# Performance work log

Measured on AMD Instinct MI355X. Metric: run time of the kernel, lower is better.

## Reference

```python
import jax, jax.numpy as jnp
import numpy as np

# Mamba2 config (matches mamba_ssm.Mamba2 defaults used by the wrapper)
D_MODEL = 1024
D_STATE = 128
D_CONV = 4
EXPAND = 2
HEADDIM = 64
CHUNK = 256
D_INNER = EXPAND * D_MODEL            # 2048
NHEADS = D_INNER // HEADDIM           # 32
CONV_DIM = D_INNER + 2 * D_STATE      # 2304 (x, B, C share the causal conv)
D_IN_PROJ = 2 * D_INNER + 2 * D_STATE + NHEADS  # z, xBC, dt
EPS = 1e-5


def rmsnorm(x, w, eps=EPS):
    return x * jax.lax.rsqrt(jnp.mean(x * x, axis=-1, keepdims=True) + eps) * w


def setup_inputs() -> dict:
    key = jax.random.key(0)
    ks = jax.random.split(key, 8)
    B, L = 2, 2048
    def w(k, shape, sc=0.02):
        return jax.random.normal(k, shape, jnp.float32) * sc
    return {
        "x": jax.random.normal(ks[0], (B, L, D_MODEL), jnp.float32),
        "norm_w": jnp.ones((D_MODEL,), jnp.float32),
        "in_proj_w": w(ks[1], (D_IN_PROJ, D_MODEL)),
        "conv_w": w(ks[2], (CONV_DIM, 1, D_CONV), 0.2),   # depthwise kernel
        "conv_b": jnp.zeros((CONV_DIM,), jnp.float32),
        "dt_bias": w(ks[3], (NHEADS,), 1.0),
        "A_log": jnp.log(1.0 + 15.0 * jax.random.uniform(ks[4], (NHEADS,), jnp.float32)),
        "D": jnp.ones((NHEADS,), jnp.float32),
        "gnorm_w": jnp.ones((D_INNER,), jnp.float32),
        "out_proj_w": w(ks[5], (D_MODEL, D_INNER)),
    }


def _ssd(xd, a, Bm, Cm):
    """Chunked SSD scan (ssd_minimal_discrete).
    xd: (b,l,h,p) = x*dt ; a: (b,l,h) = dt*A ; Bm,Cm: (b,l,n) (ngroups=1)."""
    b, l, h, p = xd.shape
    n = Bm.shape[-1]
    nc = l // CHUNK
    xd = xd.reshape(b, nc, CHUNK, h, p)
    a = a.reshape(b, nc, CHUNK, h).transpose(0, 3, 1, 2)   # (b,h,nc,c)
    Bm = Bm.reshape(b, nc, CHUNK, n)
    Cm = Cm.reshape(b, nc, CHUNK, n)
    a_cs = jnp.cumsum(a, axis=-1)                           # (b,h,nc,c)
    # 1) intra-chunk: causal decay matrix L[t,s] = exp(sum_{s<i<=t} a_i)
    diff = a_cs[..., :, None] - a_cs[..., None, :]          # (b,h,nc,c,c)
    mask = jnp.tril(jnp.ones((CHUNK, CHUNK), bool))
    Lm = jnp.exp(jnp.where(mask, diff, 0.0)) * mask
    Y_diag = jnp.einsum("bcln,bcsn,bhcls,bcshp->bclhp", Cm, Bm, Lm, xd)
    # 2) per-chunk end states
    decay_states = jnp.exp(a_cs[..., -1:] - a_cs)           # (b,h,nc,c)
    states = jnp.einsum("bcln,bhcl,bclhp->bchpn", Bm, decay_states, xd)
    # 3) inter-chunk recurrence (vectorized segsum over the 8+1 chunk totals)
    tot = jnp.pad(a_cs[..., -1], ((0, 0), (0, 0), (1, 0)))  # (b,h,nc+1)
    tot_cs = jnp.cumsum(tot, axis=-1)
    dchunk = tot_cs[..., :, None] - tot_cs[..., None, :]    # (b,h,nc+1,nc+1)
    cmask = jnp.tril(jnp.ones((nc + 1, nc + 1), bool))
    dchunk = jnp.exp(jnp.where(cmask, dchunk, 0.0)) * cmask
    states = jnp.concatenate([jnp.zeros_like(states[:, :1]), states], axis=1)
    new_states = jnp.einsum("bhzc,bchpn->bzhpn", dchunk, states)
    init_states = new_states[:, :-1]                        # state entering each chunk
    # 4) state -> output contribution
    Y_off = jnp.einsum("bcln,bchpn,bhcl->bclhp", Cm, init_states, jnp.exp(a_cs))
    return (Y_diag + Y_off).reshape(b, l, h, p)


def reference(x, norm_w, in_proj_w, conv_w, conv_b, dt_bias, A_log, D, gnorm_w, out_proj_w):
    res = x
    u = rmsnorm(x, norm_w)
    zxbcdt = u @ in_proj_w.T                                # (b,l,d_in_proj)
    z, xBC, dt = jnp.split(zxbcdt, [D_INNER, D_INNER + CONV_DIM], axis=-1)
    # causal depthwise conv1d over (x,B,C), then SiLU
    xBC_t = jnp.pad(xBC.transpose(0, 2, 1), ((0, 0), (0, 0), (D_CONV - 1, 0)))
    conv = jax.lax.conv_general_dilated(
        xBC_t, conv_w, (1,), "VALID",
        dimension_numbers=("NCH", "OIH", "NCH"), feature_group_count=CONV_DIM)
    xBC = jax.nn.silu(conv.transpose(0, 2, 1) + conv_b)
    xs, Bm, Cm = jnp.split(xBC, [D_INNER, D_INNER + D_STATE], axis=-1)
    dt = jax.nn.softplus(dt + dt_bias)                      # (b,l,h)
    A = -jnp.exp(A_log)                                     # (h,)
    xh = xs.reshape(xs.shape[0], xs.shape[1], NHEADS, HEADDIM)
    y = _ssd(xh * dt[..., None], dt * A, Bm, Cm)
    y = y + D[None, None, :, None] * xh                     # skip term
    y = y.reshape(xs.shape)
    y = rmsnorm(y * jax.nn.silu(z), gnorm_w)                # gated RMSNorm
    return res + y @ out_proj_w.T
```

## Files before the change

### kernel.cpp

```cpp
#include <hip/hip_runtime.h>
#include <hip/hip_bf16.h>

typedef __hip_bfloat16 bf16_t;
typedef __attribute__((ext_vector_type(8))) short bfrag8;
typedef __attribute__((ext_vector_type(4))) float floatx4;

#define DM     1024
#define DI     2048
#define NHD    32
#define HD     64
#define DSTATE 128
#define CONVD  2304
#define NPROJ  4384
#define NPAD   4480
#define MR     4096
#define LL     2048
#define EPSF   1e-5f
#define LOG2E  1.44269504088896f

__device__ __forceinline__ void gl_lds16(const void* g, void* l) {
  __builtin_amdgcn_global_load_lds((const __attribute__((address_space(1))) void*)g,
                                   (__attribute__((address_space(3))) void*)l, 16, 0, 0);
}
__device__ __forceinline__ unsigned pack_bf16_rn(float a, float b) {
  unsigned ua = (__float_as_uint(a) + 0x8000u) >> 16;
  unsigned ub = (__float_as_uint(b) + 0x8000u) >> 16;
  return ua | (ub << 16);
}
__device__ __forceinline__ unsigned short bf16u(float a) {
  return (unsigned short)((__float_as_uint(a) + 0x8000u) >> 16);
}
__device__ __forceinline__ float blo(unsigned u){ return __uint_as_float(u << 16); }
__device__ __forceinline__ float bhi(unsigned u){ return __uint_as_float(u & 0xffff0000u); }
__device__ __forceinline__ void unp8(uint4 u, float* v) {
  v[0]=blo(u.x); v[1]=bhi(u.x); v[2]=blo(u.y); v[3]=bhi(u.y);
  v[4]=blo(u.z); v[5]=bhi(u.z); v[6]=blo(u.w); v[7]=bhi(u.w);
}
typedef union { unsigned u[4]; bfrag8 f; } fragu;

__global__ void rms1_kernel(const float* __restrict__ x, const float* __restrict__ w,
                            bf16_t* __restrict__ ub) {
  int row = blockIdx.x, t = threadIdx.x;
  float4 v = ((const float4*)(x + (long)row * DM))[t];
  float ss = v.x*v.x + v.y*v.y + v.z*v.z + v.w*v.w;
#pragma unroll
  for (int off = 32; off > 0; off >>= 1) ss += __shfl_down(ss, off, 64);
  __shared__ float red[4];
  if ((t & 63) == 0) red[t >> 6] = ss;
  __syncthreads();
  float tot = red[0] + red[1] + red[2] + red[3];
  float rs = rsqrtf(tot * (1.f / DM) + EPSF);
  float4 wv = ((const float4*)w)[t];
  bf16_t* o = ub + (long)row * DM + t * 4;
  o[0] = __float2bfloat16(v.x * rs * wv.x);
  o[1] = __float2bfloat16(v.y * rs * wv.y);
  o[2] = __float2bfloat16(v.z * rs * wv.z);
  o[3] = __float2bfloat16(v.w * rs * wv.w);
}

#define W1CNT (NPAD * DM / 4)
#define W2CNT (DM * DI / 4)
__global__ void cvtw_kernel(const float* __restrict__ w1, const float* __restrict__ w2,
                            const float* __restrict__ gw,
                            bf16_t* __restrict__ o1, bf16_t* __restrict__ o2) {
  int i4 = blockIdx.x * 256 + threadIdx.x;
  if (i4 < W1CNT) {
    int idx = i4 * 4;
    int row = idx >> 10;
    float4 v = make_float4(0.f, 0.f, 0.f, 0.f);
    if (row < NPROJ) v = *(const float4*)(w1 + idx);
    bf16_t* d = o1 + idx;
    d[0] = __float2bfloat16(v.x); d[1] = __float2bfloat16(v.y);
    d[2] = __float2bfloat16(v.z); d[3] = __float2bfloat16(v.w);
  } else {
    int idx = (i4 - W1CNT) * 4;
    int k = idx & (DI - 1);
    float4 v = *(const float4*)(w2 + idx);
    float4 g = *(const float4*)(gw + k);
    bf16_t* d = o2 + idx;
    d[0] = __float2bfloat16(v.x * g.x); d[1] = __float2bfloat16(v.y * g.y);
    d[2] = __float2bfloat16(v.z * g.z); d[3] = __float2bfloat16(v.w * g.w);
  }
}

template<int TN, bool DO_RES, bool OUT_BF16>
__global__ __launch_bounds__(256) void gemm64_kernel(const bf16_t* __restrict__ A,
    const bf16_t* __restrict__ Bw, const float* __restrict__ resid,
    const float* __restrict__ rs_row, void* __restrict__ Cout, int N, int K) {
  __shared__ bf16_t As[128 * 64];
  __shared__ bf16_t Bs[TN * 64];
  const int tid = threadIdx.x;
  const int lane = tid & 63;
  const int wv = tid >> 6;
  const int l15 = lane & 15;
  const int l4 = lane >> 4;
  constexpr int MF = (TN == 128) ? 4 : 2;
  const int wm = (TN == 128) ? ((wv >> 1) << 6) : (wv << 5);
  const int wn = (TN == 128) ? ((wv & 1) << 6) : 0;
  const int tm = blockIdx.x << 7;
  const int tn = blockIdx.y * TN;

  floatx4 acc[MF][4];
#pragma unroll
  for (int i = 0; i < MF; i++)
#pragma unroll
    for (int j = 0; j < 4; j++) acc[i][j] = (floatx4){0.f, 0.f, 0.f, 0.f};

  const int r = tid >> 3;
  const int c8 = tid & 7;
  const int scol = ((c8 ^ (r & 7)) << 3);
  const bf16_t* Ag = A + (long)(tm + r) * K + scol;
  const bf16_t* Bg = Bw + (long)(tn + r) * K + scol;
  const int swz = l15 & 7;

  for (int k0 = 0; k0 < K; k0 += 64) {
#pragma unroll
    for (int q = 0; q < 4; q++)
      gl_lds16(Ag + (long)(q * 32) * K + k0, &As[q * 2048 + tid * 8]);
#pragma unroll
    for (int q = 0; q < TN / 32; q++)
      gl_lds16(Bg + (long)(q * 32) * K + k0, &Bs[q * 2048 + tid * 8]);
    __syncthreads();
#pragma unroll
    for (int kk = 0; kk < 2; kk++) {
      bfrag8 af[MF], bfr[4];
      const int ch = ((kk << 2) | l4) ^ swz;
#pragma unroll
      for (int j = 0; j < 4; j++)
        bfr[j] = *(const bfrag8*)&Bs[(wn + j * 16 + l15) * 64 + ch * 8];
#pragma unroll
      for (int i = 0; i < MF; i++)
        af[i] = *(const bfrag8*)&As[(wm + i * 16 + l15) * 64 + ch * 8];
#pragma unroll
      for (int i = 0; i < MF; i++)
#pragma unroll
        for (int j = 0; j < 4; j++)
          acc[i][j] = __builtin_amdgcn_mfma_f32_16x16x32_bf16(af[i], bfr[j], acc[i][j], 0, 0, 0);
    }
    __syncthreads();
  }
#pragma unroll
  for (int i = 0; i < MF; i++)
#pragma unroll
    for (int j = 0; j < 4; j++)
#pragma unroll
      for (int r2 = 0; r2 < 4; r2++) {
        int row = tm + wm + i * 16 + l4 * 4 + r2;
        int col = tn + wn + j * 16 + l15;
        float v = acc[i][j][r2];
        if (OUT_BF16) {
          ((bf16_t*)Cout)[(long)row * N + col] = __float2bfloat16(v);
        } else {
          if (DO_RES) v = v * rs_row[row] + resid[(long)row * N + col];
          ((float*)Cout)[(long)row * N + col] = v;
        }
      }
}

__global__ __launch_bounds__(512, 2) void gemm256_kernel(const bf16_t* __restrict__ A,
    const bf16_t* __restrict__ Bw, bf16_t* __restrict__ Cout) {
  __shared__ bf16_t lds[65536];
  const int t = threadIdx.x;
  const int lane = t & 63, wv = t >> 6;
  const int wm = wv >> 2, wn = wv & 3;
  const int l15 = lane & 15, l4 = lane >> 4;
  const int flat = blockIdx.x;
  const int swzb = (flat & 7) * 32 + (flat >> 3);
  const int bx = swzb & 15, by = swzb >> 4;
  const int tm = bx << 8, tn = by << 8;

  const int srow = t >> 3;
  const int scol = ((t & 7) ^ (srow & 7)) << 3;
  const bf16_t* Ag = A + (long)(tm + srow) * DM + scol;
  const bf16_t* Bg = Bw + (long)(tn + srow) * DM + scol;
  bf16_t* Asl = lds;
  bf16_t* Bsl = lds + 32768;
  const int swl = (l15 & 7) << 4;
  const int ca0 = (l4 * 16) ^ swl;
  const int ca1 = (64 + l4 * 16) ^ swl;

  floatx4 acc[8][4];
#pragma unroll
  for (int i = 0; i < 8; i++)
#pragma unroll
    for (int j = 0; j < 4; j++) acc[i][j] = (floatx4){0.f, 0.f, 0.f, 0.f};
  bfrag8 bq[8];

#define STG_A(tt, h) { \
  bf16_t* d_ = Asl + (((tt) & 1) * 2 + (h)) * 8192 + t * 8; \
  gl_lds16(Ag + (long)((h) * 128     ) * DM + (tt) * 64, d_); \
  gl_lds16(Ag + (long)((h) * 128 + 64) * DM + (tt) * 64, d_ + 4096); \
}
#define STG_B(tt, h) { \
  bf16_t* d_ = Bsl + (((tt) & 1) * 2 + (h)) * 8192 + t * 8; \
  gl_lds16(Bg + (long)((h) * 128     ) * DM + (tt) * 64, d_); \
  gl_lds16(Bg + (long)((h) * 128 + 64) * DM + (tt) * 64, d_ + 4096); \
}
#define PH(d, q, STG, WT) { \
  const char* Ah_ = (const char*)(Asl + ((d) * 2 + wm) * 8192); \
  const char* Bh_ = (const char*)(Bsl + ((d) * 2 + (wn >> 1)) * 8192); \
  if ((q) == 0) { \
    _Pragma("unroll") \
    for (int j = 0; j < 4; j++) { \
      int r_ = ((wn & 1) << 6) + j * 16 + l15; \
      bq[j * 2]     = *(const bfrag8*)(Bh_ + r_ * 128 + ca0); \
      bq[j * 2 + 1] = *(const bfrag8*)(Bh_ + r_ * 128 + ca1); \
    } \
  } \
  bfrag8 aq0, aq1, aq2, aq3; \
  { int r_ = (q) * 32 + l15; \
    aq0 = *(const bfrag8*)(Ah_ + r_ * 128 + ca0); \
    aq1 = *(const bfrag8*)(Ah_ + r_ * 128 + ca1); \
    aq2 = *(const bfrag8*)(Ah_ + (r_ + 16) * 128 + ca0); \
    aq3 = *(const bfrag8*)(Ah_ + (r_ + 16) * 128 + ca1); } \
  STG; \
  __builtin_amdgcn_s_barrier(); \
  asm volatile("s_waitcnt lgkmcnt(0)" ::: "memory"); \
  __builtin_amdgcn_s_setprio(1); \
  _Pragma("unroll") \
  for (int j = 0; j < 4; j++) { \
    acc[(q)*2  ][j] = __builtin_amdgcn_mfma_f32_16x16x32_bf16(aq0, bq[j*2],   acc[(q)*2  ][j], 0, 0, 0); \
    acc[(q)*2  ][j] = __builtin_amdgcn_mfma_f32_16x16x32_bf16(aq1, bq[j*2+1], acc[(q)*2  ][j], 0, 0, 0); \
    acc[(q)*2+1][j] = __builtin_amdgcn_mfma_f32_16x16x32_bf16(aq2, bq[j*2],   acc[(q)*2+1][j], 0, 0, 0); \
    acc[(q)*2+1][j] = __builtin_amdgcn_mfma_f32_16x16x32_bf16(aq3, bq[j*2+1], acc[(q)*2+1][j], 0, 0, 0); \
  } \
  __builtin_amdgcn_s_setprio(0); \
  WT; \
  __builtin_amdgcn_s_barrier(); \
}

  STG_A(0, 0); STG_A(0, 1); STG_B(0, 0); STG_B(0, 1);
  STG_B(1, 0); STG_B(1, 1);
  asm volatile("s_waitcnt vmcnt(4)" ::: "memory");
  __builtin_amdgcn_s_barrier();

  for (int it = 0; it < 7; ++it) {
    const int ta = 2 * it, tb = ta + 1;
    PH(0, 0, STG_A(tb, 0), {})
    PH(0, 1, STG_A(tb, 1), {})
    PH(0, 2, STG_B(ta + 2, 0), {})
    PH(0, 3, STG_B(ta + 2, 1), asm volatile("s_waitcnt vmcnt(4)" ::: "memory");)
    PH(1, 0, STG_A(ta + 2, 0), {})
    PH(1, 1, STG_A(ta + 2, 1), {})
    PH(1, 2, STG_B(tb + 2, 0), {})
    PH(1, 3, STG_B(tb + 2, 1), asm volatile("s_waitcnt vmcnt(4)" ::: "memory");)
  }
  {
    PH(0, 0, STG_A(15, 0), {})
    PH(0, 1, STG_A(15, 1), {})
    PH(0, 2, {}, {})
    PH(0, 3, {}, asm volatile("s_waitcnt vmcnt(0)" ::: "memory");)
    PH(1, 0, {}, {})
    PH(1, 1, {}, {})
    PH(1, 2, {}, {})
    PH(1, 3, {}, {})
  }
#undef PH
#undef STG_A
#undef STG_B

  const long crow = tm + wm * 128;
  const int ccol = tn + wn * 64;
#pragma unroll
  for (int qi = 0; qi < 8; qi++)
#pragma unroll
    for (int j = 0; j < 4; j++)
#pragma unroll
      for (int r2 = 0; r2 < 4; r2++) {
        long row = crow + (qi >> 1) * 32 + (qi & 1) * 16 + l4 * 4 + r2;
        int col = ccol + j * 16 + l15;
        Cout[row * NPAD + col] = __float2bfloat16(acc[qi][j][r2]);
      }
}

__global__ __launch_bounds__(256) void gemm_s_kernel(const bf16_t* __restrict__ Cmh,
                const bf16_t* __restrict__ Bmh, float* __restrict__ SL) {
  __shared__ bf16_t As[128 * 32];
  __shared__ bf16_t Bs[128 * 32];
  const int tid = threadIdx.x;
  const int lane = tid & 63;
  const int wv = tid >> 6;
  const int wm = (wv >> 1) << 6;
  const int wn = (wv & 1) << 6;
  const int bc = blockIdx.z;
  const int tm = blockIdx.x << 7;
  const int tn = blockIdx.y << 7;
  const int l15 = lane & 15;
  const int l4 = lane >> 4;
  floatx4 acc[4][4];
#pragma unroll
  for (int i = 0; i < 4; i++)
#pragma unroll
    for (int j = 0; j < 4; j++) acc[i][j] = (floatx4){0.f, 0.f, 0.f, 0.f};
  const int arow = tid >> 2;
  const int acol = (tid & 3) << 3;
  const bf16_t* Ag = Cmh + (long)bc * 256 * DSTATE + (long)(tm + arow) * DSTATE + acol;
  const bf16_t* Bg = Bmh + (long)bc * 256 * DSTATE + (long)(tn + arow) * DSTATE + acol;
  const long k64 = (long)64 * DSTATE;
  for (int k0 = 0; k0 < DSTATE; k0 += 32) {
    gl_lds16(Ag + k0, &As[tid * 8]);
    gl_lds16(Ag + k64 + k0, &As[2048 + tid * 8]);
    gl_lds16(Bg + k0, &Bs[tid * 8]);
    gl_lds16(Bg + k64 + k0, &Bs[2048 + tid * 8]);
    __syncthreads();
    bfrag8 af[4], bfr[4];
#pragma unroll
    for (int i = 0; i < 4; i++)
      af[i] = *(const bfrag8*)&As[(wm + i * 16 + l15) * 32 + l4 * 8];
#pragma unroll
    for (int j = 0; j < 4; j++)
      bfr[j] = *(const bfrag8*)&Bs[(wn + j * 16 + l15) * 32 + l4 * 8];
#pragma unroll
    for (int i = 0; i < 4; i++)
#pragma unroll
      for (int j = 0; j < 4; j++)
        acc[i][j] = __builtin_amdgcn_mfma_f32_16x16x32_bf16(af[i], bfr[j], acc[i][j], 0, 0, 0);
    __syncthreads();
  }
  float* Cb = SL + (long)bc * 65536;
#pragma unroll
  for (int i = 0; i < 4; i++)
#pragma unroll
    for (int j = 0; j < 4; j++)
#pragma unroll
      for (int r = 0; r < 4; r++)
        Cb[(long)(tm + wm + i * 16 + l4 * 4 + r) * 256 + tn + wn + j * 16 + l15] = acc[i][j][r];
}

__global__ __launch_bounds__(256) void conv4_kernel(const bf16_t* __restrict__ zxh,
    const float* __restrict__ cw, const float* __restrict__ cb,
    bf16_t* __restrict__ xhb, bf16_t* __restrict__ Bmh, bf16_t* __restrict__ Cmh) {
  int g = blockIdx.x * 256 + threadIdx.x;
  int cg = g % 288;
  int blt = g / 288;
  int c0 = cg * 8;
  long bl0 = (long)blt * 4;
  int l0 = (int)(bl0 & (LL - 1));
  const bf16_t* base = zxh + bl0 * NPAD + DI + c0;
  float rv[7][8];
#pragma unroll
  for (int j = 0; j < 7; j++) {
    int dj = j - 3;
    if (l0 + dj >= 0) {
      uint4 u = *(const uint4*)(base + (long)dj * NPAD);
      unp8(u, rv[j]);
    } else {
#pragma unroll
      for (int q = 0; q < 8; q++) rv[j][q] = 0.f;
    }
  }
  float4 wq[8];
#pragma unroll
  for (int q = 0; q < 8; q++) wq[q] = ((const float4*)cw)[c0 + q];
  float bias[8];
  *(float4*)&bias[0] = *(const float4*)(cb + c0);
  *(float4*)&bias[4] = *(const float4*)(cb + c0 + 4);
#pragma unroll
  for (int i = 0; i < 4; i++) {
    unsigned o[4];
#pragma unroll
    for (int q2 = 0; q2 < 4; q2++) {
      float rr[2];
#pragma unroll
      for (int e = 0; e < 2; e++) {
        int q = q2 * 2 + e;
        float a = bias[q] + wq[q].x * rv[i][q] + wq[q].y * rv[i + 1][q]
                + wq[q].z * rv[i + 2][q] + wq[q].w * rv[i + 3][q];
        rr[e] = a / (1.f + __expf(-a));
      }
      o[q2] = pack_bf16_rn(rr[0], rr[1]);
    }
    uint4 ov = make_uint4(o[0], o[1], o[2], o[3]);
    long bl = bl0 + i;
    if (c0 < DI)               *(uint4*)(xhb + bl * DI + c0) = ov;
    else if (c0 < DI + DSTATE) *(uint4*)(Bmh + bl * DSTATE + (c0 - DI)) = ov;
    else                       *(uint4*)(Cmh + bl * DSTATE + (c0 - DI - DSTATE)) = ov;
  }
}

__global__ __launch_bounds__(256) void xdt_kernel(const bf16_t* __restrict__ xhb,
    const bf16_t* __restrict__ Bmh, const bf16_t* __restrict__ zxh,
    const float* __restrict__ A_log, const float* __restrict__ dtb,
    float* __restrict__ acs, float* __restrict__ ctot,
    bf16_t* __restrict__ xdT, bf16_t* __restrict__ xdTe, bf16_t* __restrict__ BmT) {
  __shared__ unsigned short Tb[9216];
  __shared__ float acsL[256];
  __shared__ float dtsL[256];
  __shared__ float wsum[4];
  int blk = blockIdx.x;
  int t = threadIdx.x;
  if (blk < 512) {
    int h = blk & 31, bc = blk >> 5;
    {
      int lane = t & 63, w = t >> 6;
      float Ah = -__expf(A_log[h]) * LOG2E;
      int gl = bc * 256 + t;
      float vv = __bfloat162float(zxh[(long)gl * NPAD + (NPROJ - 32) + h]) + dtb[h];
      float sp = fmaxf(vv, 0.f) + log1pf(__expf(-fabsf(vv)));
      float a = sp * Ah;
#pragma unroll
      for (int off = 1; off < 64; off <<= 1) {
        float v = __shfl_up(a, off, 64);
        if (lane >= off) a += v;
      }
      if (lane == 63) wsum[w] = a;
      __syncthreads();
      float base = 0.f;
      for (int i = 0; i < 4; i++) base += (i < w) ? wsum[i] : 0.f;
      a += base;
      acsL[t] = a;
      dtsL[t] = sp;
      acs[blk * 256 + t] = a;
      if (t == 255) ctot[blk] = a;
      __syncthreads();
    }
    float atot = acsL[255];
    unsigned short* T1 = Tb;
    unsigned short* T2 = Tb + 4608;
    int l_loc = t >> 2, pg = t & 3;
    for (int lt = 0; lt < 4; lt++) {
      int ll = lt * 64 + l_loc;
      int gl = bc * 256 + ll;
      float w1 = dtsL[ll];
      float w2 = w1 * exp2f(atot - acsL[ll]);
      const uint4* src = (const uint4*)(xhb + (long)gl * DI + h * HD + pg * 16);
      uint4 u0 = src[0], u1 = src[1];
      float v[16];
      unp8(u0, v); unp8(u1, v + 8);
      __syncthreads();
#pragma unroll
      for (int q = 0; q < 16; q++) {
        T1[(pg * 16 + q) * 72 + l_loc] = bf16u(v[q] * w1);
        T2[(pg * 16 + q) * 72 + l_loc] = bf16u(v[q] * w2);
      }
      __syncthreads();
      long orow = ((long)blk * 64 + l_loc) * 256 + lt * 64 + pg * 16;
      *(uint4*)(xdT + orow)      = *(uint4*)&T1[l_loc * 72 + pg * 16];
      *(uint4*)(xdT + orow + 8)  = *(uint4*)&T1[l_loc * 72 + pg * 16 + 8];
      *(uint4*)(xdTe + orow)     = *(uint4*)&T2[l_loc * 72 + pg * 16];
      *(uint4*)(xdTe + orow + 8) = *(uint4*)&T2[l_loc * 72 + pg * 16 + 8];
    }
  } else {
    unsigned short* T = Tb;
    int bc = blk - 512;
    int l_loc = t >> 2, ng = t & 3;
    for (int lt = 0; lt < 4; lt++) {
      int gl = bc * 256 + lt * 64 + l_loc;
      const uint4* src = (const uint4*)(Bmh + (long)gl * DSTATE + ng * 32);
      uint4 u[4];
#pragma unroll
      for (int q = 0; q < 4; q++) u[q] = src[q];
      __syncthreads();
      const unsigned short* us = (const unsigned short*)u;
#pragma unroll
      for (int e = 0; e < 32; e++)
        T[(ng * 32 + e) * 72 + l_loc] = us[e];
      __syncthreads();
      int n = t >> 1, lg2 = t & 1;
      long orow = ((long)bc * 128 + n) * 256 + lt * 64 + lg2 * 32;
#pragma unroll
      for (int q = 0; q < 4; q++)
        *(uint4*)(BmT + orow + q * 8) = *(uint4*)&T[n * 72 + lg2 * 32 + q * 8];
    }
  }
}

__global__ __launch_bounds__(256) void states3_kernel(const bf16_t* __restrict__ xdTe,
    const bf16_t* __restrict__ BmT, bf16_t* __restrict__ states) {
  int blk = blockIdx.x;
  int bc = blk >> 5;
  int t = threadIdx.x, lane = t & 63, wv = t >> 6;
  int l15 = lane & 15, l4 = lane >> 4;
  floatx4 acc[2][4];
#pragma unroll
  for (int i = 0; i < 2; i++)
#pragma unroll
    for (int j = 0; j < 4; j++) acc[i][j] = (floatx4){0.f, 0.f, 0.f, 0.f};
  const bf16_t* arow = BmT + (long)bc * 128 * 256;
  const bf16_t* brow = xdTe + (long)blk * 64 * 256;
#pragma unroll
  for (int kt = 0; kt < 8; kt++) {
    bfrag8 af[2], bfr[4];
#pragma unroll
    for (int i = 0; i < 2; i++)
      af[i] = *(const bfrag8*)(arow + (long)(wv * 32 + i * 16 + l15) * 256 + kt * 32 + l4 * 8);
#pragma unroll
    for (int j = 0; j < 4; j++)
      bfr[j] = *(const bfrag8*)(brow + (long)(j * 16 + l15) * 256 + kt * 32 + l4 * 8);
#pragma unroll
    for (int i = 0; i < 2; i++)
#pragma unroll
      for (int j = 0; j < 4; j++)
        acc[i][j] = __builtin_amdgcn_mfma_f32_16x16x32_bf16(af[i], bfr[j], acc[i][j], 0, 0, 0);
  }
#pragma unroll
  for (int i = 0; i < 2; i++)
#pragma unroll
    for (int j = 0; j < 4; j++) {
      int n_base = wv * 32 + i * 16 + l4 * 4;
      int p = j * 16 + l15;
      unsigned lo = pack_bf16_rn(acc[i][j][0], acc[i][j][1]);
      unsigned hi = pack_bf16_rn(acc[i][j][2], acc[i][j][3]);
      *(uint2*)(states + (long)blk * 8192 + p * 128 + n_base) = make_uint2(lo, hi);
    }
}

__global__ void scan_kernel(const bf16_t* __restrict__ states, const float* __restrict__ ctot,
                            bf16_t* __restrict__ initsb) {
  int id = blockIdx.x * 256 + threadIdx.x;
  int pn = id & 8191;
  int bh = id >> 13;
  int b = bh >> 5, h = bh & 31;
  float S = 0.f;
#pragma unroll
  for (int c = 0; c < 8; c++) {
    int blk = (b * 8 + c) * 32 + h;
    initsb[(long)blk * 8192 + pn] = __float2bfloat16(S);
    S = exp2f(ctot[blk]) * S + __bfloat162float(states[(long)blk * 8192 + pn]);
  }
}

__global__ __launch_bounds__(512, 4) void yk4_kernel(const float* __restrict__ SL,
     const bf16_t* __restrict__ Cmh, const bf16_t* __restrict__ xhb,
     const bf16_t* __restrict__ zxh, const float* __restrict__ acs,
     const bf16_t* __restrict__ initsb, const bf16_t* __restrict__ xdT,
     const float* __restrict__ Dp, bf16_t* __restrict__ yg, float* __restrict__ ssqp) {
  int bi = blockIdx.x;
  int bc = (bi & 7) * 2 + ((bi >> 3) & 1);
  int h = bi >> 4;
  int ablk = bc * 32 + h;
  int t = threadIdx.x;
  int wv = t >> 6;
  int mh = wv >> 2, wsub = wv & 3;
  int lane = t & 63;
  int l15 = lane & 15, l4 = lane >> 4;

  __shared__ float acsS[256];
  __shared__ __align__(16) char bbuf[49152];
  bf16_t* xds = (bf16_t*)bbuf;
  bf16_t* ins = (bf16_t*)(bbuf + 32768);
  float* Yt = (float*)bbuf;

  {
    const bf16_t* xrow_g = xdT + (long)ablk * 64 * 256;
#pragma unroll
    for (int it = 0; it < 4; it++) {
      int sl = it * 512 + t;
      int p = sl >> 5, s = sl & 31;
      int c = (s & 24) | ((s & 7) ^ (p & 7));
      gl_lds16(xrow_g + p * 256 + c * 8, &xds[sl * 8]);
    }
    const bf16_t* irow_g = initsb + (long)ablk * 8192;
#pragma unroll
    for (int it = 0; it < 2; it++) {
      int sl = it * 512 + t;
      int p = sl >> 4, s = sl & 15;
      int c = (s & 8) | ((s & 7) ^ (p & 7));
      gl_lds16(irow_g + p * 128 + c * 8, &ins[sl * 8]);
    }
  }
  if (t < 256) acsS[t] = acs[ablk * 256 + t];
  __syncthreads();

  const int rowbase = bc * 256;
  const int l0 = mh * 128 + wsub * 32 + l15;
  const int l1 = l0 + 16;
  const float al0 = acsS[l0], al1 = acsS[l1];
  const float eA0 = exp2f(al0), eA1 = exp2f(al1);
  const float* SL0 = SL + (long)bc * 65536 + (long)l0 * 256;
  const float* SL1 = SL + (long)bc * 65536 + (long)l1 * 256;

  floatx4 acc[2][4];
#pragma unroll
  for (int i = 0; i < 2; i++)
#pragma unroll
    for (int j = 0; j < 4; j++) acc[i][j] = (floatx4){0.f, 0.f, 0.f, 0.f};

  const int nkd = (mh + 1) * 4;
  for (int kt = 0; kt < nkd; kt++) {
    int sbase = kt * 32 + l4 * 8;
    float as[8];
    *(float4*)&as[0] = *(const float4*)&acsS[sbase];
    *(float4*)&as[4] = *(const float4*)&acsS[sbase + 4];
    float sv0[8], sv1[8];
    *(float4*)&sv0[0] = *(const float4*)(SL0 + sbase);
    *(float4*)&sv0[4] = *(const float4*)(SL0 + sbase + 4);
    *(float4*)&sv1[0] = *(const float4*)(SL1 + sbase);
    *(float4*)&sv1[4] = *(const float4*)(SL1 + sbase + 4);
    fragu af0, af1;
#pragma unroll
    for (int q2 = 0; q2 < 4; q2++) {
      float p00, p01, p10, p11;
      {
        int s = sbase + q2 * 2;
        float d0 = al0 - as[q2 * 2], d1 = al0 - as[q2 * 2 + 1];
        p00 = (s <= l0) ? sv0[q2 * 2] * exp2f(fminf(d0, 0.f)) : 0.f;
        p01 = (s + 1 <= l0) ? sv0[q2 * 2 + 1] * exp2f(fminf(d1, 0.f)) : 0.f;
        float e0 = al1 - as[q2 * 2], e1 = al1 - as[q2 * 2 + 1];
        p10 = (s <= l1) ? sv1[q2 * 2] * exp2f(fminf(e0, 0.f)) : 0.f;
        p11 = (s + 1 <= l1) ? sv1[q2 * 2 + 1] * exp2f(fminf(e1, 0.f)) : 0.f;
      }
      af0.u[q2] = pack_bf16_rn(p00, p01);
      af1.u[q2] = pack_bf16_rn(p10, p11);
    }
    bfrag8 bfr[4];
    int ch = kt * 4 + l4;
#pragma unroll
    for (int j = 0; j < 4; j++) {
      int p = j * 16 + l15;
      int sw = (ch & 24) | ((ch & 7) ^ (p & 7));
      bfr[j] = *(const bfrag8*)&xds[(p * 32 + sw) * 8];
    }
#pragma unroll
    for (int j = 0; j < 4; j++) {
      acc[0][j] = __builtin_amdgcn_mfma_f32_16x16x32_bf16(af0.f, bfr[j], acc[0][j], 0, 0, 0);
      acc[1][j] = __builtin_amdgcn_mfma_f32_16x16x32_bf16(af1.f, bfr[j], acc[1][j], 0, 0, 0);
    }
  }
#pragma unroll
  for (int kt = 0; kt < 4; kt++) {
    int n0 = kt * 32 + l4 * 8;
    uint4 c0 = *(const uint4*)(Cmh + (long)(rowbase + l0) * DSTATE + n0);
    uint4 c1 = *(const uint4*)(Cmh + (long)(rowbase + l1) * DSTATE + n0);
    float cv0[8], cv1[8];
    unp8(c0, cv0); unp8(c1, cv1);
    fragu af0, af1;
#pragma unroll
    for (int q2 = 0; q2 < 4; q2++) {
      af0.u[q2] = pack_bf16_rn(cv0[q2 * 2] * eA0, cv0[q2 * 2 + 1] * eA0);
      af1.u[q2] = pack_bf16_rn(cv1[q2 * 2] * eA1, cv1[q2 * 2 + 1] * eA1);
    }
    bfrag8 bfr[4];
    int ch = kt * 4 + l4;
#pragma unroll
    for (int j = 0; j < 4; j++) {
      int p = j * 16 + l15;
      int sw = (ch & 8) | ((ch & 7) ^ (p & 7));
      bfr[j] = *(const bfrag8*)&ins[(p * 16 + sw) * 8];
    }
#pragma unroll
    for (int j = 0; j < 4; j++) {
      acc[0][j] = __builtin_amdgcn_mfma_f32_16x16x32_bf16(af0.f, bfr[j], acc[0][j], 0, 0, 0);
      acc[1][j] = __builtin_amdgcn_mfma_f32_16x16x32_bf16(af1.f, bfr[j], acc[1][j], 0, 0, 0);
    }
  }
  float Dh = Dp[h];
#pragma unroll
  for (int pass = 0; pass < 2; pass++) {
    __syncthreads();
    if (mh == pass) {
#pragma unroll
      for (int i = 0; i < 2; i++)
#pragma unroll
        for (int j = 0; j < 4; j++)
#pragma unroll
          for (int r = 0; r < 4; r++)
            Yt[(wsub * 32 + i * 16 + l4 * 4 + r) * 66 + j * 16 + l15] = acc[i][j][r];
    }
    __syncthreads();
    {
      int row_l = t >> 2;
      int chc = (t & 3) * 16;
      long rowg = rowbase + pass * 128 + row_l;
      float ss = 0.f;
#pragma unroll
      for (int it = 0; it < 2; it++) {
        int c = chc + it * 8;
        float4 y0 = *(const float4*)&Yt[row_l * 66 + c];
        float4 y1 = *(const float4*)&Yt[row_l * 66 + c + 4];
        uint4 ux = *(const uint4*)(xhb + rowg * DI + h * HD + c);
        uint4 uz = *(const uint4*)(zxh + rowg * NPAD + h * HD + c);
        float xv[8], zv[8];
        unp8(ux, xv); unp8(uz, zv);
        float yv[8] = {y0.x, y0.y, y0.z, y0.w, y1.x, y1.y, y1.z, y1.w};
        unsigned o[4];
#pragma unroll
        for (int q = 0; q < 4; q++) {
          float v0 = (yv[q * 2 + 0] + Dh * xv[q * 2 + 0]) *
                     (zv[q * 2 + 0] / (1.f + __expf(-zv[q * 2 + 0])));
          float v1 = (yv[q * 2 + 1] + Dh * xv[q * 2 + 1]) *
                     (zv[q * 2 + 1] / (1.f + __expf(-zv[q * 2 + 1])));
          ss += v0 * v0 + v1 * v1;
          o[q] = pack_bf16_rn(v0, v1);
        }
        *(uint4*)(yg + rowg * DI + h * HD + c) = make_uint4(o[0], o[1], o[2], o[3]);
      }
      ss += __shfl_xor(ss, 1, 64);
      ss += __shfl_xor(ss, 2, 64);
      if ((t & 3) == 0) ssqp[rowg * 32 + h] = ss;
    }
  }
}

__global__ void rsred_kernel(const float* __restrict__ ssqp, float* __restrict__ rs) {
  int row = blockIdx.x * 256 + threadIdx.x;
  const float4* p = (const float4*)(ssqp + row * 32);
  float s = 0.f;
#pragma unroll
  for (int q = 0; q < 8; q++) {
    float4 v = p[q];
    s += v.x + v.y + v.z + v.w;
  }
  rs[row] = rsqrtf(s * (1.f / DI) + EPSF);
}

extern "C" void kernel_launch(void* const* d_in, const int* in_sizes, int n_in,
                              void* d_out, int out_size, void* d_ws, size_t ws_size,
                              hipStream_t stream) {
  const float* x    = (const float*)d_in[0];
  const float* nw   = (const float*)d_in[1];
  const float* w1   = (const float*)d_in[2];
  const float* cw   = (const float*)d_in[3];
  const float* cb   = (const float*)d_in[4];
  const float* dtb  = (const float*)d_in[5];
  const float* alog = (const float*)d_in[6];
  const float* Dp   = (const float*)d_in[7];
  const float* gw   = (const float*)d_in[8];
  const float* w2   = (const float*)d_in[9];
  float* out = (float*)d_out;

  char* ws = (char*)d_ws;
  size_t off = 0;
  auto alloc = [&](size_t bytes) -> void* {
    void* p = ws + off;
    off += (bytes + 255) & ~(size_t)255;
    return p;
  };
  bf16_t* ub     = (bf16_t*)alloc((size_t)MR * DM * 2);
  bf16_t* w1b    = (bf16_t*)alloc((size_t)NPAD * DM * 2);
  bf16_t* w2b    = (bf16_t*)alloc((size_t)DM * DI * 2);
  bf16_t* zxh    = (bf16_t*)alloc((size_t)MR * NPAD * 2);
  bf16_t* xhb    = (bf16_t*)alloc((size_t)MR * DI * 2);
  bf16_t* Bmh    = (bf16_t*)alloc((size_t)MR * DSTATE * 2);
  bf16_t* Cmh    = (bf16_t*)alloc((size_t)MR * DSTATE * 2);
  float* SL      = (float*)alloc((size_t)16 * 256 * 256 * 4);
  float* acs     = (float*)alloc((size_t)512 * 256 * 4);
  float* ctot    = (float*)alloc((size_t)512 * 4);
  bf16_t* states = (bf16_t*)alloc((size_t)512 * 8192 * 2);
  bf16_t* initsb = (bf16_t*)alloc((size_t)512 * 8192 * 2);
  bf16_t* xdT    = (bf16_t*)alloc((size_t)512 * 64 * 256 * 2);
  bf16_t* xdTe   = (bf16_t*)alloc((size_t)512 * 64 * 256 * 2);
  bf16_t* BmT    = (bf16_t*)alloc((size_t)16 * 128 * 256 * 2);
  bf16_t* yg     = (bf16_t*)alloc((size_t)MR * DI * 2);
  float* ssqp    = (float*)alloc((size_t)MR * NHD * 4);
  float* rs      = (float*)alloc((size_t)MR * 4);
  if (off > ws_size) return;

  rms1_kernel<<<MR, 256, 0, stream>>>(x, nw, ub);
  cvtw_kernel<<<(W1CNT + W2CNT) / 256, 256, 0, stream>>>(w1, w2, gw, w1b, w2b);
  gemm256_kernel<<<256, 512, 0, stream>>>(ub, w1b, zxh);
  gemm64_kernel<64, false, true><<<dim3(MR / 128, 6), 256, 0, stream>>>(
      ub, w1b + (size_t)4096 * DM, nullptr, nullptr, zxh + 4096, NPAD, DM);
  conv4_kernel<<<(1024 * 288) / 256, 256, 0, stream>>>(zxh, cw, cb, xhb, Bmh, Cmh);
  xdt_kernel<<<528, 256, 0, stream>>>(xhb, Bmh, zxh, alog, dtb, acs, ctot, xdT, xdTe, BmT);
  gemm_s_kernel<<<dim3(2, 2, 16), 256, 0, stream>>>(Cmh, Bmh, SL);
  states3_kernel<<<512, 256, 0, stream>>>(xdTe, BmT, states);
  scan_kernel<<<(2 * 32 * 8192) / 256, 256, 0, stream>>>(states, ctot, initsb);
  yk4_kernel<<<512, 512, 0, stream>>>(SL, Cmh, xhb, zxh, acs, initsb, xdT, Dp, yg, ssqp);
  rsred_kernel<<<MR / 256, 256, 0, stream>>>(ssqp, rs);
  gemm64_kernel<64, true, false><<<dim3(MR / 128, DM / 64), 256, 0, stream>>>(
      yg, w2b, x, rs, out, DM, DI);
}
```

Before: 263.7 us.

## Merge small kernels, fold rms reduction into out-proj GEMM, retile GEMMs

Merges rmsnorm with the weight conversion, and the states GEMM with the C·B score GEMM, each into a single launch. The gated-RMSNorm row reduction moves into the out-projection GEMM prologue, which removes the separate reduction kernel. Both small GEMMs switch to 128-wide N tiles, and the main GEMM gets a new XCD-aware block mapping. The aim is to cut launch count and gaps between launches and to improve cache locality, at the cost of fewer blocks in the retiled GEMMs. Each out-proj block now recomputes the row reduction redundantly.

```diff
diff --git a/kernel.cpp b/kernel.cpp
--- a/kernel.cpp
+++ b/kernel.cpp
@@ -38,57 +38,61 @@
 }
 typedef union { unsigned u[4]; bfrag8 f; } fragu;
 
-__global__ void rms1_kernel(const float* __restrict__ x, const float* __restrict__ w,
-                            bf16_t* __restrict__ ub) {
-  int row = blockIdx.x, t = threadIdx.x;
-  float4 v = ((const float4*)(x + (long)row * DM))[t];
-  float ss = v.x*v.x + v.y*v.y + v.z*v.z + v.w*v.w;
-#pragma unroll
-  for (int off = 32; off > 0; off >>= 1) ss += __shfl_down(ss, off, 64);
-  __shared__ float red[4];
-  if ((t & 63) == 0) red[t >> 6] = ss;
-  __syncthreads();
-  float tot = red[0] + red[1] + red[2] + red[3];
-  float rs = rsqrtf(tot * (1.f / DM) + EPSF);
-  float4 wv = ((const float4*)w)[t];
-  bf16_t* o = ub + (long)row * DM + t * 4;
-  o[0] = __float2bfloat16(v.x * rs * wv.x);
-  o[1] = __float2bfloat16(v.y * rs * wv.y);
-  o[2] = __float2bfloat16(v.z * rs * wv.z);
-  o[3] = __float2bfloat16(v.w * rs * wv.w);
-}
-
 #define W1CNT (NPAD * DM / 4)
 #define W2CNT (DM * DI / 4)
-__global__ void cvtw_kernel(const float* __restrict__ w1, const float* __restrict__ w2,
-                            const float* __restrict__ gw,
-                            bf16_t* __restrict__ o1, bf16_t* __restrict__ o2) {
-  int i4 = blockIdx.x * 256 + threadIdx.x;
-  if (i4 < W1CNT) {
-    int idx = i4 * 4;
-    int row = idx >> 10;
-    float4 v = make_float4(0.f, 0.f, 0.f, 0.f);
-    if (row < NPROJ) v = *(const float4*)(w1 + idx);
-    bf16_t* d = o1 + idx;
-    d[0] = __float2bfloat16(v.x); d[1] = __float2bfloat16(v.y);
-    d[2] = __float2bfloat16(v.z); d[3] = __float2bfloat16(v.w);
+#define CVTBLK ((W1CNT + W2CNT) / 256)
+__global__ void rms_cvt_kernel(const float* __restrict__ x, const float* __restrict__ w,
+                               bf16_t* __restrict__ ub,
+                               const float* __restrict__ w1, const float* __restrict__ w2,
+                               const float* __restrict__ gw,
+                               bf16_t* __restrict__ o1, bf16_t* __restrict__ o2) {
+  __shared__ float red[4];
+  int t = threadIdx.x;
+  if (blockIdx.x < MR) {
+    int row = blockIdx.x;
+    float4 v = ((const float4*)(x + (long)row * DM))[t];
+    float ss = v.x*v.x + v.y*v.y + v.z*v.z + v.w*v.w;
+#pragma unroll
+    for (int off = 32; off > 0; off >>= 1) ss += __shfl_down(ss, off, 64);
+    if ((t & 63) == 0) red[t >> 6] = ss;
+    __syncthreads();
+    float tot = red[0] + red[1] + red[2] + red[3];
+    float rs = rsqrtf(tot * (1.f / DM) + EPSF);
+    float4 wv = ((const float4*)w)[t];
+    bf16_t* o = ub + (long)row * DM + t * 4;
+    o[0] = __float2bfloat16(v.x * rs * wv.x);
+    o[1] = __float2bfloat16(v.y * rs * wv.y);
+    o[2] = __float2bfloat16(v.z * rs * wv.z);
+    o[3] = __float2bfloat16(v.w * rs * wv.w);
   } else {
-    int idx = (i4 - W1CNT) * 4;
-    int k = idx & (DI - 1);
-    float4 v = *(const float4*)(w2 + idx);
-    float4 g = *(const float4*)(gw + k);
-    bf16_t* d = o2 + idx;
-    d[0] = __float2bfloat16(v.x * g.x); d[1] = __float2bfloat16(v.y * g.y);
-    d[2] = __float2bfloat16(v.z * g.z); d[3] = __float2bfloat16(v.w * g.w);
+    int i4 = (blockIdx.x - MR) * 256 + t;
+    if (i4 < W1CNT) {
+      int idx = i4 * 4;
+      int row = idx >> 10;
+      float4 v = make_float4(0.f, 0.f, 0.f, 0.f);
+      if (row < NPROJ) v = *(const float4*)(w1 + idx);
+      bf16_t* d = o1 + idx;
+      d[0] = __float2bfloat16(v.x); d[1] = __float2bfloat16(v.y);
+      d[2] = __float2bfloat16(v.z); d[3] = __float2bfloat16(v.w);
+    } else {
+      int idx = (i4 - W1CNT) * 4;
+      int k = idx & (DI - 1);
+      float4 v = *(const float4*)(w2 + idx);
+      float4 g = *(const float4*)(gw + k);
+      bf16_t* d = o2 + idx;
+      d[0] = __float2bfloat16(v.x * g.x); d[1] = __float2bfloat16(v.y * g.y);
+      d[2] = __float2bfloat16(v.z * g.z); d[3] = __float2bfloat16(v.w * g.w);
+    }
   }
 }
 
 template<int TN, bool DO_RES, bool OUT_BF16>
 __global__ __launch_bounds__(256) void gemm64_kernel(const bf16_t* __restrict__ A,
     const bf16_t* __restrict__ Bw, const float* __restrict__ resid,
-    const float* __restrict__ rs_row, void* __restrict__ Cout, int N, int K) {
+    const float* __restrict__ ssqp, void* __restrict__ Cout, int N, int K) {
   __shared__ bf16_t As[128 * 64];
   __shared__ bf16_t Bs[TN * 64];
+  __shared__ float rsS[128];
   const int tid = threadIdx.x;
   const int lane = tid & 63;
   const int wv = tid >> 6;
@@ -100,6 +104,16 @@
   const int tm = blockIdx.x << 7;
   const int tn = blockIdx.y * TN;
 
+  if (DO_RES) {
+    int rr = tid >> 1;
+    const float4* pp = (const float4*)(ssqp + (long)(tm + rr) * 32 + (tid & 1) * 16);
+    float s = 0.f;
+#pragma unroll
+    for (int q = 0; q < 4; q++) { float4 v = pp[q]; s += v.x + v.y + v.z + v.w; }
+    s += __shfl_xor(s, 1, 64);
+    if ((tid & 1) == 0) rsS[rr] = rsqrtf(s * (1.f / DI) + EPSF);
+  }
+
   floatx4 acc[MF][4];
 #pragma unroll
   for (int i = 0; i < MF; i++)
@@ -151,7 +165,7 @@
         if (OUT_BF16) {
           ((bf16_t*)Cout)[(long)row * N + col] = __float2bfloat16(v);
         } else {
-          if (DO_RES) v = v * rs_row[row] + resid[(long)row * N + col];
+          if (DO_RES) v = v * rsS[row - tm] + resid[(long)row * N + col];
           ((float*)Cout)[(long)row * N + col] = v;
         }
       }
@@ -164,9 +178,9 @@
   const int lane = t & 63, wv = t >> 6;
   const int wm = wv >> 2, wn = wv & 3;
   const int l15 = lane & 15, l4 = lane >> 4;
-  const int flat = blockIdx.x;
-  const int swzb = (flat & 7) * 32 + (flat >> 3);
-  const int bx = swzb & 15, by = swzb >> 4;
+  const int xcd = blockIdx.x & 7, idx = blockIdx.x >> 3;
+  const int bx = (xcd & 3) * 4 + (idx & 3);
+  const int by = (xcd >> 2) * 8 + (idx >> 2);
   const int tm = bx << 8, tn = by << 8;
 
   const int srow = t >> 3;
@@ -273,58 +287,95 @@
       }
 }
 
-__global__ __launch_bounds__(256) void gemm_s_kernel(const bf16_t* __restrict__ Cmh,
-                const bf16_t* __restrict__ Bmh, float* __restrict__ SL) {
+__global__ __launch_bounds__(256) void sst_kernel(const bf16_t* __restrict__ xdTe,
+    const bf16_t* __restrict__ BmT, bf16_t* __restrict__ states,
+    const bf16_t* __restrict__ Cmh, const bf16_t* __restrict__ Bmh,
+    float* __restrict__ SL) {
   __shared__ bf16_t As[128 * 32];
   __shared__ bf16_t Bs[128 * 32];
-  const int tid = threadIdx.x;
-  const int lane = tid & 63;
-  const int wv = tid >> 6;
-  const int wm = (wv >> 1) << 6;
-  const int wn = (wv & 1) << 6;
-  const int bc = blockIdx.z;
-  const int tm = blockIdx.x << 7;
-  const int tn = blockIdx.y << 7;
-  const int l15 = lane & 15;
-  const int l4 = lane >> 4;
-  floatx4 acc[4][4];
-#pragma unroll
-  for (int i = 0; i < 4; i++)
-#pragma unroll
-    for (int j = 0; j < 4; j++) acc[i][j] = (floatx4){0.f, 0.f, 0.f, 0.f};
-  const int arow = tid >> 2;
-  const int acol = (tid & 3) << 3;
-  const bf16_t* Ag = Cmh + (long)bc * 256 * DSTATE + (long)(tm + arow) * DSTATE + acol;
-  const bf16_t* Bg = Bmh + (long)bc * 256 * DSTATE + (long)(tn + arow) * DSTATE + acol;
-  const long k64 = (long)64 * DSTATE;
-  for (int k0 = 0; k0 < DSTATE; k0 += 32) {
-    gl_lds16(Ag + k0, &As[tid * 8]);
-    gl_lds16(Ag + k64 + k0, &As[2048 + tid * 8]);
-    gl_lds16(Bg + k0, &Bs[tid * 8]);
-    gl_lds16(Bg + k64 + k0, &Bs[2048 + tid * 8]);
-    __syncthreads();
-    bfrag8 af[4], bfr[4];
+  const int t = threadIdx.x, lane = t & 63, wv = t >> 6;
+  const int l15 = lane & 15, l4 = lane >> 4;
+  if (blockIdx.x < 512) {
+    int blk = blockIdx.x;
+    int bc = blk >> 5;
+    floatx4 acc[2][4];
+#pragma unroll
+    for (int i = 0; i < 2; i++)
+#pragma unroll
+      for (int j = 0; j < 4; j++) acc[i][j] = (floatx4){0.f, 0.f, 0.f, 0.f};
+    const bf16_t* arow = BmT + (long)bc * 128 * 256;
+    const bf16_t* brow = xdTe + (long)blk * 64 * 256;
+#pragma unroll
+    for (int kt = 0; kt < 8; kt++) {
+      bfrag8 af[2], bfr[4];
+#pragma unroll
+      for (int i = 0; i < 2; i++)
+        af[i] = *(const bfrag8*)(arow + (long)(wv * 32 + i * 16 + l15) * 256 + kt * 32 + l4 * 8);
+#pragma unroll
+      for (int j = 0; j < 4; j++)
+        bfr[j] = *(const bfrag8*)(brow + (long)(j * 16 + l15) * 256 + kt * 32 + l4 * 8);
+#pragma unroll
+      for (int i = 0; i < 2; i++)
+#pragma unroll
+        for (int j = 0; j < 4; j++)
+          acc[i][j] = __builtin_amdgcn_mfma_f32_16x16x32_bf16(af[i], bfr[j], acc[i][j], 0, 0, 0);
+    }
+#pragma unroll
+    for (int i = 0; i < 2; i++)
+#pragma unroll
+      for (int j = 0; j < 4; j++) {
+        int n_base = wv * 32 + i * 16 + l4 * 4;
+        int p = j * 16 + l15;
+        unsigned lo = pack_bf16_rn(acc[i][j][0], acc[i][j][1]);
+        unsigned hi = pack_bf16_rn(acc[i][j][2], acc[i][j][3]);
+        *(uint2*)(states + (long)blk * 8192 + p * 128 + n_base) = make_uint2(lo, hi);
+      }
+  } else {
+    int idx = blockIdx.x - 512;
+    const int bc = idx >> 2;
+    const int tm = ((idx >> 1) & 1) << 7;
+    const int tn = (idx & 1) << 7;
+    const int wm = (wv >> 1) << 6;
+    const int wn = (wv & 1) << 6;
+    floatx4 acc[4][4];
 #pragma unroll
     for (int i = 0; i < 4; i++)
-      af[i] = *(const bfrag8*)&As[(wm + i * 16 + l15) * 32 + l4 * 8];
-#pragma unroll
-    for (int j = 0; j < 4; j++)
-      bfr[j] = *(const bfrag8*)&Bs[(wn + j * 16 + l15) * 32 + l4 * 8];
+#pragma unroll
+      for (int j = 0; j < 4; j++) acc[i][j] = (floatx4){0.f, 0.f, 0.f, 0.f};
+    const int arow = t >> 2;
+    const int acol = (t & 3) << 3;
+    const bf16_t* Ag = Cmh + (long)bc * 256 * DSTATE + (long)(tm + arow) * DSTATE + acol;
+    const bf16_t* Bg = Bmh + (long)bc * 256 * DSTATE + (long)(tn + arow) * DSTATE + acol;
+    const long k64 = (long)64 * DSTATE;
+    for (int k0 = 0; k0 < DSTATE; k0 += 32) {
+      gl_lds16(Ag + k0, &As[t * 8]);
+      gl_lds16(Ag + k64 + k0, &As[2048 + t * 8]);
+      gl_lds16(Bg + k0, &Bs[t * 8]);
+      gl_lds16(Bg + k64 + k0, &Bs[2048 + t * 8]);
+      __syncthreads();
+      bfrag8 af[4], bfr[4];
+#pragma unroll
+      for (int i = 0; i < 4; i++)
+        af[i] = *(const bfrag8*)&As[(wm + i * 16 + l15) * 32 + l4 * 8];
+#pragma unroll
+      for (int j = 0; j < 4; j++)
+        bfr[j] = *(const bfrag8*)&Bs[(wn + j * 16 + l15) * 32 + l4 * 8];
+#pragma unroll
+      for (int i = 0; i < 4; i++)
+#pragma unroll
+        for (int j = 0; j < 4; j++)
+          acc[i][j] = __builtin_amdgcn_mfma_f32_16x16x32_bf16(af[i], bfr[j], acc[i][j], 0, 0, 0);
+      __syncthreads();
+    }
+    float* Cb = SL + (long)bc * 65536;
 #pragma unroll
     for (int i = 0; i < 4; i++)
 #pragma unroll
       for (int j = 0; j < 4; j++)
-        acc[i][j] = __builtin_amdgcn_mfma_f32_16x16x32_bf16(af[i], bfr[j], acc[i][j], 0, 0, 0);
-    __syncthreads();
-  }
-  float* Cb = SL + (long)bc * 65536;
-#pragma unroll
-  for (int i = 0; i < 4; i++)
-#pragma unroll
-    for (int j = 0; j < 4; j++)
-#pragma unroll
-      for (int r = 0; r < 4; r++)
-        Cb[(long)(tm + wm + i * 16 + l4 * 4 + r) * 256 + tn + wn + j * 16 + l15] = acc[i][j][r];
+#pragma unroll
+        for (int r = 0; r < 4; r++)
+          Cb[(long)(tm + wm + i * 16 + l4 * 4 + r) * 256 + tn + wn + j * 16 + l15] = acc[i][j][r];
+  }
 }
 
 __global__ __launch_bounds__(256) void conv4_kernel(const bf16_t* __restrict__ zxh,
@@ -465,46 +516,6 @@
   }
 }
 
-__global__ __launch_bounds__(256) void states3_kernel(const bf16_t* __restrict__ xdTe,
-    const bf16_t* __restrict__ BmT, bf16_t* __restrict__ states) {
-  int blk = blockIdx.x;
-  int bc = blk >> 5;
-  int t = threadIdx.x, lane = t & 63, wv = t >> 6;
-  int l15 = lane & 15, l4 = lane >> 4;
-  floatx4 acc[2][4];
-#pragma unroll
-  for (int i = 0; i < 2; i++)
-#pragma unroll
-    for (int j = 0; j < 4; j++) acc[i][j] = (floatx4){0.f, 0.f, 0.f, 0.f};
-  const bf16_t* arow = BmT + (long)bc * 128 * 256;
-  const bf16_t* brow = xdTe + (long)blk * 64 * 256;
-#pragma unroll
-  for (int kt = 0; kt < 8; kt++) {
-    bfrag8 af[2], bfr[4];
-#pragma unroll
-    for (int i = 0; i < 2; i++)
-      af[i] = *(const bfrag8*)(arow + (long)(wv * 32 + i * 16 + l15) * 256 + kt * 32 + l4 * 8);
-#pragma unroll
-    for (int j = 0; j < 4; j++)
-      bfr[j] = *(const bfrag8*)(brow + (long)(j * 16 + l15) * 256 + kt * 32 + l4 * 8);
-#pragma unroll
-    for (int i = 0; i < 2; i++)
-#pragma unroll
-      for (int j = 0; j < 4; j++)
-        acc[i][j] = __builtin_amdgcn_mfma_f32_16x16x32_bf16(af[i], bfr[j], acc[i][j], 0, 0, 0);
-  }
-#pragma unroll
-  for (int i = 0; i < 2; i++)
-#pragma unroll
-    for (int j = 0; j < 4; j++) {
-      int n_base = wv * 32 + i * 16 + l4 * 4;
-      int p = j * 16 + l15;
-      unsigned lo = pack_bf16_rn(acc[i][j][0], acc[i][j][1]);
-      unsigned hi = pack_bf16_rn(acc[i][j][2], acc[i][j][3]);
-      *(uint2*)(states + (long)blk * 8192 + p * 128 + n_base) = make_uint2(lo, hi);
-    }
-}
-
 __global__ void scan_kernel(const bf16_t* __restrict__ states, const float* __restrict__ ctot,
                             bf16_t* __restrict__ initsb) {
   int id = blockIdx.x * 256 + threadIdx.x;
@@ -690,18 +701,6 @@
       if ((t & 3) == 0) ssqp[rowg * 32 + h] = ss;
     }
   }
-}
-
-__global__ void rsred_kernel(const float* __restrict__ ssqp, float* __restrict__ rs) {
-  int row = blockIdx.x * 256 + threadIdx.x;
-  const float4* p = (const float4*)(ssqp + row * 32);
-  float s = 0.f;
-#pragma unroll
-  for (int q = 0; q < 8; q++) {
-    float4 v = p[q];
-    s += v.x + v.y + v.z + v.w;
-  }
-  rs[row] = rsqrtf(s * (1.f / DI) + EPSF);
 }
 
 extern "C" void kernel_launch(void* const* d_in, const int* in_sizes, int n_in,
@@ -743,21 +742,17 @@
   bf16_t* BmT    = (bf16_t*)alloc((size_t)16 * 128 * 256 * 2);
   bf16_t* yg     = (bf16_t*)alloc((size_t)MR * DI * 2);
   float* ssqp    = (float*)alloc((size_t)MR * NHD * 4);
-  float* rs      = (float*)alloc((size_t)MR * 4);
   if (off > ws_size) return;
 
-  rms1_kernel<<<MR, 256, 0, stream>>>(x, nw, ub);
-  cvtw_kernel<<<(W1CNT + W2CNT) / 256, 256, 0, stream>>>(w1, w2, gw, w1b, w2b);
+  rms_cvt_kernel<<<MR + CVTBLK, 256, 0, stream>>>(x, nw, ub, w1, w2, gw, w1b, w2b);
   gemm256_kernel<<<256, 512, 0, stream>>>(ub, w1b, zxh);
-  gemm64_kernel<64, false, true><<<dim3(MR / 128, 6), 256, 0, stream>>>(
+  gemm64_kernel<128, false, true><<<dim3(MR / 128, 3), 256, 0, stream>>>(
       ub, w1b + (size_t)4096 * DM, nullptr, nullptr, zxh + 4096, NPAD, DM);
   conv4_kernel<<<(1024 * 288) / 256, 256, 0, stream>>>(zxh, cw, cb, xhb, Bmh, Cmh);
   xdt_kernel<<<528, 256, 0, stream>>>(xhb, Bmh, zxh, alog, dtb, acs, ctot, xdT, xdTe, BmT);
-  gemm_s_kernel<<<dim3(2, 2, 16), 256, 0, stream>>>(Cmh, Bmh, SL);
-  states3_kernel<<<512, 256, 0, stream>>>(xdTe, BmT, states);
+  sst_kernel<<<576, 256, 0, stream>>>(xdTe, BmT, states, Cmh, Bmh, SL);
   scan_kernel<<<(2 * 32 * 8192) / 256, 256, 0, stream>>>(states, ctot, initsb);
   yk4_kernel<<<512, 512, 0, stream>>>(SL, Cmh, xhb, zxh, acs, initsb, xdT, Dp, yg, ssqp);
-  rsred_kernel<<<MR / 256, 256, 0, stream>>>(ssqp, rs);
-  gemm64_kernel<64, true, false><<<dim3(MR / 128, DM / 64), 256, 0, stream>>>(
-      yg, w2b, x, rs, out, DM, DI);
-}
+  gemm64_kernel<128, true, false><<<dim3(MR / 128, DM / 128), 256, 0, stream>>>(
+      yg, w2b, x, ssqp, out, DM, DI);
+}
```

New measurement: 270.8 us. 2.7% more time.
